# Optimization experiments

Hardware: AMD Instinct MI355X
Metric: run time of the kernel (lower is better)

The kernel has to match this reference:

```python
import jax, jax.numpy as jnp
import numpy as np

N, C, H, W = 8, 32, 16, 16   # input batch / channels / spatial
OC = 64                       # out_channels
K = 3                         # kernel_size
PAD = 1                       # padding (stride=1, dilation=1 -> output HxW == input HxW)
WIDTH = 8                     # hwcfg['width']
RLEN = 2 ** WIDTH             # Sobol RNG sequence length = 256
CKK = C * K * K               # unfolded patch length = 288
B = N * H * W                 # flattened patch batch = 2048


def _sobol_rng():
    # 1-D Sobol sequence == van der Corput base-2: bit-reversed counter scaled to [0, 2^width)
    idx = np.arange(RLEN, dtype=np.uint32)
    rev = np.zeros(RLEN, dtype=np.uint32)
    for b in range(WIDTH):
        rev |= ((idx >> b) & 1) << (WIDTH - 1 - b)
    return jnp.asarray(rev.astype(np.float32))


def setup_inputs() -> dict:
    key = jax.random.key(0)
    k1, k2, k3, k4, k5, k6 = jax.random.split(key, 6)
    # unary (stochastic bitstream) input: bits in {0,1}
    x = jax.random.bernoulli(k1, 0.5, (N, C, H, W)).astype(jnp.float32)
    # BinGen, bipolar: binary = round((v + 1)/2 * 2^width), v in [-1, 1]
    w = jax.random.uniform(k2, (OC, CKK), minval=-1.0, maxval=1.0)
    w_bin = jnp.round((w + 1.0) / 2.0 * RLEN)
    b = jax.random.uniform(k3, (OC,), minval=-1.0, maxval=1.0)
    b_bin = jnp.round((b + 1.0) / 2.0 * RLEN)
    rng = _sobol_rng()
    # mid-stream BSGen index state (per patch position, as the module cats to batch copies)
    wrdx_i1 = jax.random.randint(k4, (B, OC, CKK), 0, RLEN, dtype=jnp.int32)
    wrdx_i0 = jax.random.randint(k5, (B, OC, CKK), 0, RLEN, dtype=jnp.int32)
    brdx = jax.random.randint(k6, (OC,), 0, RLEN, dtype=jnp.int32)
    return {"x": x, "w_bin": w_bin, "b_bin": b_bin, "rng": rng,
            "wrdx_i1": wrdx_i1, "wrdx_i0": wrdx_i0, "brdx": brdx}


def _unfold(x):
    # even cycle -> ConstantPad2d(pad, 0); torch.nn.functional.unfold ordering (c, kh, kw)
    xp = jnp.pad(x, ((0, 0), (0, 0), (PAD, PAD), (PAD, PAD)))
    cols = jnp.stack([xp[:, :, i:i + H, j:j + W] for i in range(K) for j in range(K)], axis=2)
    # [N, C, K*K, H, W] -> [N, CKK, L] -> [N, L, CKK] -> [B, CKK]
    return cols.reshape(N, CKK, H * W).transpose(0, 2, 1).reshape(B, CKK)


def reference(x, w_bin, b_bin, rng, wrdx_i1, wrdx_i0, brdx):
    ib1 = _unfold(x)                                                        # [B, CKK], bits
    # BSGen: bit = (binary_value > rng[index % RLEN])
    wbit1 = (w_bin[None] > rng[wrdx_i1 % RLEN]).astype(jnp.float32)         # [B, OC, CKK]
    wbit0 = 1.0 - (w_bin[None] > rng[wrdx_i0 % RLEN]).astype(jnp.float32)   # [B, OC, CKK]
    # bipolar parallel counter: x*w1 path + (1-x)*(1-w) path
    obin = (jnp.einsum('bk,bok->bo', ib1, wbit1)
            + jnp.einsum('bk,bok->bo', 1.0 - ib1, wbit0))                   # [B, OC]
    bbit = (b_bin > rng[brdx % RLEN]).astype(jnp.float32)                   # [OC]
    # fold(1,1): [N, L, OC] -> [N, OC, H, W]
    out = obin.reshape(N, H * W, OC).transpose(0, 2, 1).reshape(N, OC, H, W)
    return out + bbit[None, :, None, None]
```

## Files before the change

### kernel.cpp

```cpp
#include <hip/hip_runtime.h>


#define CH   32
#define HH   16
#define WW   16
#define OCN  64
#define CKK  288
#define LL   256
#define BB   2048

#define WS_XM_OFF 0
#define WS_WK_OFF 131072
#define WS_BB_OFF 204800

__device__ __forceinline__ float unf_val(const float* __restrict__ x,
                                         int n, int h, int w0, int k) {
    int c  = k / 9;
    int r  = k - c * 9;
    int kh = r / 3;
    int kw = r - kh * 3;
    int ih = h + kh - 1;
    int iw = w0 + kw - 1;
    float v = 0.f;
    if ((unsigned)ih < 16u && (unsigned)iw < 16u)
        v = x[((n * CH + c) * HH + ih) * WW + iw];
    return v;
}

__global__ __launch_bounds__(256) void fsu_pre(
    const float* __restrict__ x, const float* __restrict__ w_bin,
    const float* __restrict__ b_bin, const int* __restrict__ brdx,
    unsigned long long* __restrict__ xm, unsigned* __restrict__ wk,
    float* __restrict__ bb)
{
    if (blockIdx.x == 512) {
        for (int i = threadIdx.x; i < OCN * CKK; i += 256) {
            unsigned wi = (unsigned)w_bin[i];
            wk[i] = (wi >= 256u) ? 0xFFFFFFFFu : (wi << 24);
        }
        if (threadIdx.x < OCN) {
            int o = threadIdx.x;
            float rv = (float)(__brev((unsigned)brdx[o]) >> 24);
            bb[o] = (b_bin[o] > rv) ? 1.f : 0.f;
        }
        return;
    }
    const int wave = threadIdx.x >> 6;
    const int lane = threadIdx.x & 63;
    const int b = blockIdx.x * 4 + wave;
    const int n = b >> 8, l = b & 255;
    const int h = l >> 4, w0 = l & 15;

    unsigned long long m[8];
    #pragma unroll
    for (int e = 0; e < 4; ++e)
        m[e] = __ballot(unf_val(x, n, h, w0, lane * 4 + e) != 0.f);
    #pragma unroll
    for (int e = 0; e < 4; ++e)
        m[4 + e] = __ballot(unf_val(x, n, h, w0, 256 + (lane & 7) * 4 + e) != 0.f);

    if (lane == 0) {
        #pragma unroll
        for (int e = 0; e < 8; ++e) xm[(size_t)b * 8 + e] = m[e];
    }
}

struct Row {
    int4  a, c;
    uint4 k;
    int4  at, ct;
    uint4 kt;
};

__device__ __forceinline__ void load_row(Row& r, const int* __restrict__ p1,
                                         const int* __restrict__ p0,
                                         const unsigned* __restrict__ pw,
                                         int j, int lane, int tl) {
    const int4*  q1 = (const int4*)(p1 + j * CKK);
    const int4*  q0 = (const int4*)(p0 + j * CKK);
    const uint4* qw = (const uint4*)(pw + j * CKK);
    r.a  = q1[lane]; r.c  = q0[lane]; r.k  = qw[lane];
    r.at = q1[tl];   r.ct = q0[tl];   r.kt = qw[tl];
}

__device__ __forceinline__ unsigned long long chunkm(unsigned k, int a1, int a0,
                                                     unsigned long long xm) {
    unsigned long long m1 = __ballot(k > __brev((unsigned)a1));
    unsigned long long m0 = __ballot(k > __brev((unsigned)a0));
    return (xm & m1) | (~xm & ~m0);
}

__global__ __launch_bounds__(256) void fsu_stream(
    const int* __restrict__ wrdx1, const int* __restrict__ wrdx0,
    const unsigned* __restrict__ wk, const unsigned long long* __restrict__ xm,
    const float* __restrict__ bb, float* __restrict__ out)
{
    const int blk  = blockIdx.x;
    const int b    = blk >> 2;
    const int og   = blk & 3;
    const int wave = threadIdx.x >> 6;
    const int lane = threadIdx.x & 63;
    const int obase = og * 16 + wave * 4;
    const int n = b >> 8, l = b & 255;
    const int tl = 64 + (lane & 7);

    const unsigned long long* xb = xm + (size_t)b * 8;
    const unsigned long long xm0 = xb[0], xm1 = xb[1], xm2 = xb[2], xm3 = xb[3];
    const unsigned long long xt0 = xb[4], xt1 = xb[5], xt2 = xb[6], xt3 = xb[7];

    const int* p1 = wrdx1 + ((size_t)b * OCN + obase) * CKK;
    const int* p0 = wrdx0 + ((size_t)b * OCN + obase) * CKK;
    const unsigned* pw = wk + (size_t)obase * CKK;
    float* po = out + ((size_t)n * OCN + obase) * LL + l;

    auto docompute = [&](const Row& r, int j) {
        unsigned cnt = 0;
        cnt += __popcll(chunkm(r.k.x,  r.a.x,  r.c.x,  xm0));
        cnt += __popcll(chunkm(r.k.y,  r.a.y,  r.c.y,  xm1));
        cnt += __popcll(chunkm(r.k.z,  r.a.z,  r.c.z,  xm2));
        cnt += __popcll(chunkm(r.k.w,  r.a.w,  r.c.w,  xm3));
        cnt += __popcll(chunkm(r.kt.x, r.at.x, r.ct.x, xt0) & 0xFFull);
        cnt += __popcll(chunkm(r.kt.y, r.at.y, r.ct.y, xt1) & 0xFFull);
        cnt += __popcll(chunkm(r.kt.z, r.at.z, r.ct.z, xt2) & 0xFFull);
        cnt += __popcll(chunkm(r.kt.w, r.at.w, r.ct.w, xt3) & 0xFFull);
        if (lane == 0)
            po[j * LL] = (float)cnt + bb[obase + j];
    };

    Row A, B;
    load_row(A, p1, p0, pw, 0, lane, tl);
    load_row(B, p1, p0, pw, 1, lane, tl);
    __builtin_amdgcn_sched_barrier(0);
    docompute(A, 0);
    load_row(A, p1, p0, pw, 2, lane, tl);
    __builtin_amdgcn_sched_barrier(0);
    docompute(B, 1);
    load_row(B, p1, p0, pw, 3, lane, tl);
    __builtin_amdgcn_sched_barrier(0);
    docompute(A, 2);
    docompute(B, 3);
}

extern "C" void kernel_launch(void* const* d_in, const int* in_sizes, int n_in,
                              void* d_out, int out_size, void* d_ws, size_t ws_size,
                              hipStream_t stream) {
    const float* x     = (const float*)d_in[0];
    const float* w_bin = (const float*)d_in[1];
    const float* b_bin = (const float*)d_in[2];
    const int*   wrdx1 = (const int*)d_in[4];
    const int*   wrdx0 = (const int*)d_in[5];
    const int*   brdx  = (const int*)d_in[6];
    float*       out   = (float*)d_out;

    unsigned long long* xm = (unsigned long long*)((char*)d_ws + WS_XM_OFF);
    unsigned*           wk = (unsigned*)((char*)d_ws + WS_WK_OFF);
    float*              bb = (float*)((char*)d_ws + WS_BB_OFF);

    fsu_pre<<<dim3(513), dim3(256), 0, stream>>>(x, w_bin, b_bin, brdx, xm, wk, bb);
    fsu_stream<<<dim3(BB * 4), dim3(256), 0, stream>>>(wrdx1, wrdx0, wk, xm, bb, out);
}
```

Baseline: 330.2 us.

## Stream index rows via async global-to-LDS loads with per-wave double buffering

Reorganises fsu_stream so each wave owns one output channel and iterates over 16 patches. Weight keys and the bias bit are computed once in registers, and the index rows are streamed into LDS through global_load_lds with a two-buffer pipeline gated by vmcnt waits. The weight and bias preprocessing moves out of fsu_pre, and the grid shrinks from 8192 to 2048 blocks. The aim is to overlap HBM loads of the large wrdx arrays with the ballot and popcount work and to cut per-block setup, at the cost of hand-tuned waitcnt ordering and fewer resident blocks.

```diff
diff --git a/kernel.cpp b/kernel.cpp
--- a/kernel.cpp
+++ b/kernel.cpp
@@ -8,10 +8,25 @@
 #define CKK  288
 #define LL   256
 #define BB   2048
+#define BPW  16
+#define ROWSTRIDE (OCN * CKK)
 
-#define WS_XM_OFF 0
-#define WS_WK_OFF 131072
-#define WS_BB_OFF 204800
+__device__ __forceinline__ unsigned wkey(float wv) {
+    unsigned wi = (unsigned)wv;
+    return (wi >= 256u) ? 0xFFFFFFFFu : (wi << 24);
+}
+
+__device__ __forceinline__ void async16(const void* g, void* l) {
+    __builtin_amdgcn_global_load_lds(
+        (const __attribute__((address_space(1))) void*)g,
+        (__attribute__((address_space(3))) void*)l, 16, 0, 0);
+}
+
+__device__ __forceinline__ unsigned long long rfl64(unsigned long long v) {
+    unsigned lo = __builtin_amdgcn_readfirstlane((unsigned)v);
+    unsigned hi = __builtin_amdgcn_readfirstlane((unsigned)(v >> 32));
+    return ((unsigned long long)hi << 32) | lo;
+}
 
 __device__ __forceinline__ float unf_val(const float* __restrict__ x,
                                          int n, int h, int w0, int k) {
@@ -28,23 +43,8 @@
 }
 
 __global__ __launch_bounds__(256) void fsu_pre(
-    const float* __restrict__ x, const float* __restrict__ w_bin,
-    const float* __restrict__ b_bin, const int* __restrict__ brdx,
-    unsigned long long* __restrict__ xm, unsigned* __restrict__ wk,
-    float* __restrict__ bb)
+    const float* __restrict__ x, unsigned long long* __restrict__ xm)
 {
-    if (blockIdx.x == 512) {
-        for (int i = threadIdx.x; i < OCN * CKK; i += 256) {
-            unsigned wi = (unsigned)w_bin[i];
-            wk[i] = (wi >= 256u) ? 0xFFFFFFFFu : (wi << 24);
-        }
-        if (threadIdx.x < OCN) {
-            int o = threadIdx.x;
-            float rv = (float)(__brev((unsigned)brdx[o]) >> 24);
-            bb[o] = (b_bin[o] > rv) ? 1.f : 0.f;
-        }
-        return;
-    }
     const int wave = threadIdx.x >> 6;
     const int lane = threadIdx.x & 63;
     const int b = blockIdx.x * 4 + wave;
@@ -65,24 +65,6 @@
     }
 }
 
-struct Row {
-    int4  a, c;
-    uint4 k;
-    int4  at, ct;
-    uint4 kt;
-};
-
-__device__ __forceinline__ void load_row(Row& r, const int* __restrict__ p1,
-                                         const int* __restrict__ p0,
-                                         const unsigned* __restrict__ pw,
-                                         int j, int lane, int tl) {
-    const int4*  q1 = (const int4*)(p1 + j * CKK);
-    const int4*  q0 = (const int4*)(p0 + j * CKK);
-    const uint4* qw = (const uint4*)(pw + j * CKK);
-    r.a  = q1[lane]; r.c  = q0[lane]; r.k  = qw[lane];
-    r.at = q1[tl];   r.ct = q0[tl];   r.kt = qw[tl];
-}
-
 __device__ __forceinline__ unsigned long long chunkm(unsigned k, int a1, int a0,
                                                      unsigned long long xm) {
     unsigned long long m1 = __ballot(k > __brev((unsigned)a1));
@@ -92,53 +74,97 @@
 
 __global__ __launch_bounds__(256) void fsu_stream(
     const int* __restrict__ wrdx1, const int* __restrict__ wrdx0,
-    const unsigned* __restrict__ wk, const unsigned long long* __restrict__ xm,
-    const float* __restrict__ bb, float* __restrict__ out)
+    const float* __restrict__ w_bin, const float* __restrict__ b_bin,
+    const int* __restrict__ brdx,
+    const unsigned long long* __restrict__ xm,
+    float* __restrict__ out)
 {
-    const int blk  = blockIdx.x;
-    const int b    = blk >> 2;
-    const int og   = blk & 3;
+    __shared__ __align__(16) int buf[4][2][2 * CKK];
+    __shared__ __align__(16) unsigned long long xml[BPW * 8];
+
     const int wave = threadIdx.x >> 6;
     const int lane = threadIdx.x & 63;
-    const int obase = og * 16 + wave * 4;
-    const int n = b >> 8, l = b & 255;
-    const int tl = 64 + (lane & 7);
+    const int og   = blockIdx.x & 15;
+    const int bch  = blockIdx.x >> 4;
+    const int o    = og * 4 + wave;
+    const int b0   = bch * BPW;
 
-    const unsigned long long* xb = xm + (size_t)b * 8;
-    const unsigned long long xm0 = xb[0], xm1 = xb[1], xm2 = xb[2], xm3 = xb[3];
-    const unsigned long long xt0 = xb[4], xt1 = xb[5], xt2 = xb[6], xt3 = xb[7];
+    const float* pw = w_bin + (size_t)o * CKK;
+    float4 wm = ((const float4*)pw)[lane];
+    float4 wt = ((const float4*)pw)[64 + (lane & 7)];
+    uint4 km = make_uint4(wkey(wm.x), wkey(wm.y), wkey(wm.z), wkey(wm.w));
+    uint4 kt = make_uint4(wkey(wt.x), wkey(wt.y), wkey(wt.z), wkey(wt.w));
+    float bbv = (b_bin[o] > (float)(__brev((unsigned)brdx[o]) >> 24)) ? 1.f : 0.f;
 
-    const int* p1 = wrdx1 + ((size_t)b * OCN + obase) * CKK;
-    const int* p0 = wrdx0 + ((size_t)b * OCN + obase) * CKK;
-    const unsigned* pw = wk + (size_t)obase * CKK;
-    float* po = out + ((size_t)n * OCN + obase) * LL + l;
+    if (wave == 0)
+        async16((const char*)(xm + (size_t)b0 * 8) + lane * 16,
+                (char*)xml);
+    __syncthreads();
 
-    auto docompute = [&](const Row& r, int j) {
-        unsigned cnt = 0;
-        cnt += __popcll(chunkm(r.k.x,  r.a.x,  r.c.x,  xm0));
-        cnt += __popcll(chunkm(r.k.y,  r.a.y,  r.c.y,  xm1));
-        cnt += __popcll(chunkm(r.k.z,  r.a.z,  r.c.z,  xm2));
-        cnt += __popcll(chunkm(r.k.w,  r.a.w,  r.c.w,  xm3));
-        cnt += __popcll(chunkm(r.kt.x, r.at.x, r.ct.x, xt0) & 0xFFull);
-        cnt += __popcll(chunkm(r.kt.y, r.at.y, r.ct.y, xt1) & 0xFFull);
-        cnt += __popcll(chunkm(r.kt.z, r.at.z, r.ct.z, xt2) & 0xFFull);
-        cnt += __popcll(chunkm(r.kt.w, r.at.w, r.ct.w, xt3) & 0xFFull);
-        if (lane == 0)
-            po[j * LL] = (float)cnt + bb[obase + j];
+    int* bufA = &buf[wave][0][0];
+    int* bufB = &buf[wave][1][0];
+
+    const int* g1 = wrdx1 + ((size_t)b0 * OCN + o) * CKK + lane * 4;
+    const int* g0 = wrdx0 + ((size_t)b0 * OCN + o) * CKK + lane * 4;
+    const int* t1 = wrdx1 + ((size_t)b0 * OCN + o) * CKK + 256 + (lane & 7) * 4;
+    const int* t0 = wrdx0 + ((size_t)b0 * OCN + o) * CKK + 256 + (lane & 7) * 4;
+
+    auto issue = [&](int j, int* dst) {
+        __builtin_amdgcn_sched_barrier(0);
+        async16(g1 + (size_t)j * ROWSTRIDE, dst);
+        async16(g0 + (size_t)j * ROWSTRIDE, dst + CKK);
+        if (lane < 8) {
+            async16(t1 + (size_t)j * ROWSTRIDE, (char*)dst + 1024);
+            async16(t0 + (size_t)j * ROWSTRIDE, (char*)dst + 4 * CKK + 1024);
+        }
     };
 
-    Row A, B;
-    load_row(A, p1, p0, pw, 0, lane, tl);
-    load_row(B, p1, p0, pw, 1, lane, tl);
-    __builtin_amdgcn_sched_barrier(0);
-    docompute(A, 0);
-    load_row(A, p1, p0, pw, 2, lane, tl);
-    __builtin_amdgcn_sched_barrier(0);
-    docompute(B, 1);
-    load_row(B, p1, p0, pw, 3, lane, tl);
-    __builtin_amdgcn_sched_barrier(0);
-    docompute(A, 2);
-    docompute(B, 3);
+    auto compute = [&](const int* src, int j) {
+        const unsigned long long* xr = xml + j * 8;
+        unsigned long long x0 = rfl64(xr[0]), x1 = rfl64(xr[1]);
+        unsigned long long x2 = rfl64(xr[2]), x3 = rfl64(xr[3]);
+        unsigned long long y0 = rfl64(xr[4]), y1 = rfl64(xr[5]);
+        unsigned long long y2 = rfl64(xr[6]), y3 = rfl64(xr[7]);
+
+        int4 a  = *(const int4*)((const char*)src + lane * 16);
+        int4 at = *(const int4*)((const char*)src + 1024 + (lane & 7) * 16);
+        int4 c  = *(const int4*)((const char*)src + 4 * CKK + lane * 16);
+        int4 ct = *(const int4*)((const char*)src + 4 * CKK + 1024 + (lane & 7) * 16);
+
+        unsigned cnt = 0;
+        cnt += __popcll(chunkm(km.x, a.x, c.x, x0));
+        cnt += __popcll(chunkm(km.y, a.y, c.y, x1));
+        cnt += __popcll(chunkm(km.z, a.z, c.z, x2));
+        cnt += __popcll(chunkm(km.w, a.w, c.w, x3));
+        cnt += __popcll(chunkm(kt.x, at.x, ct.x, y0) & 0xFFull);
+        cnt += __popcll(chunkm(kt.y, at.y, ct.y, y1) & 0xFFull);
+        cnt += __popcll(chunkm(kt.z, at.z, ct.z, y2) & 0xFFull);
+        cnt += __popcll(chunkm(kt.w, at.w, ct.w, y3) & 0xFFull);
+
+        if (lane == 0) {
+            int bcur = b0 + j;
+            int n = bcur >> 8, l = bcur & 255;
+            out[((size_t)n * OCN + o) * LL + l] = (float)cnt + bbv;
+        }
+    };
+
+    issue(0, bufA);
+    #pragma unroll
+    for (int p = 0; p < 8; ++p) {
+        const int j = p * 2;
+        issue(j + 1, bufB);
+        asm volatile("s_waitcnt vmcnt(4)" ::: "memory");
+        __builtin_amdgcn_sched_barrier(0);
+        compute(bufA, j);
+        if (p < 7) {
+            issue(j + 2, bufA);
+            asm volatile("s_waitcnt vmcnt(4)" ::: "memory");
+        } else {
+            asm volatile("s_waitcnt vmcnt(0)" ::: "memory");
+        }
+        __builtin_amdgcn_sched_barrier(0);
+        compute(bufB, j + 1);
+    }
 }
 
 extern "C" void kernel_launch(void* const* d_in, const int* in_sizes, int n_in,
@@ -152,10 +178,9 @@
     const int*   brdx  = (const int*)d_in[6];
     float*       out   = (float*)d_out;
 
-    unsigned long long* xm = (unsigned long long*)((char*)d_ws + WS_XM_OFF);
-    unsigned*           wk = (unsigned*)((char*)d_ws + WS_WK_OFF);
-    float*              bb = (float*)((char*)d_ws + WS_BB_OFF);
+    unsigned long long* xm = (unsigned long long*)d_ws;
 
-    fsu_pre<<<dim3(513), dim3(256), 0, stream>>>(x, w_bin, b_bin, brdx, xm, wk, bb);
-    fsu_stream<<<dim3(BB * 4), dim3(256), 0, stream>>>(wrdx1, wrdx0, wk, xm, bb, out);
+    fsu_pre<<<dim3(BB / 4), dim3(256), 0, stream>>>(x, xm);
+    fsu_stream<<<dim3(BB), dim3(256), 0, stream>>>(wrdx1, wrdx0, w_bin, b_bin,
+                                                   brdx, xm, out);
 }
```

New measurement: 324.5 us. No clear change (-1.7%).

## Stream index rows through LDS with async global-to-LDS loads, one block per patch

Applied to the files above, without the earlier changes.

The streaming kernel now runs one block per patch, with each wave handling 16 output channels. Index rows are staged into LDS with global_load_lds in a 4-deep ring buffer, and s_waitcnt vmcnt controls when each slot is read. Weights are stored as 16-bit values and copied once per block into LDS, and the comparison moves to the 8-bit domain. The goal is to keep more bytes in flight on what is a bandwidth-bound read of two 150MB index tensors, at the cost of larger LDS use and fragile hand-written waitcnt accounting.

```diff
diff --git a/kernel.cpp b/kernel.cpp
--- a/kernel.cpp
+++ b/kernel.cpp
@@ -6,12 +6,20 @@
 #define WW   16
 #define OCN  64
 #define CKK  288
+#define CKKB 1152
 #define LL   256
 #define BB   2048
+#define DEPTH 4
 
 #define WS_XM_OFF 0
 #define WS_WK_OFF 131072
-#define WS_BB_OFF 204800
+#define WS_BB_OFF 167936
+
+__device__ __forceinline__ void async16(const void* g, void* l) {
+    __builtin_amdgcn_global_load_lds(
+        (const __attribute__((address_space(1))) void*)g,
+        (__attribute__((address_space(3))) void*)l, 16, 0, 0);
+}
 
 __device__ __forceinline__ float unf_val(const float* __restrict__ x,
                                          int n, int h, int w0, int k) {
@@ -30,14 +38,12 @@
 __global__ __launch_bounds__(256) void fsu_pre(
     const float* __restrict__ x, const float* __restrict__ w_bin,
     const float* __restrict__ b_bin, const int* __restrict__ brdx,
-    unsigned long long* __restrict__ xm, unsigned* __restrict__ wk,
+    unsigned long long* __restrict__ xm, unsigned short* __restrict__ wk16,
     float* __restrict__ bb)
 {
     if (blockIdx.x == 512) {
-        for (int i = threadIdx.x; i < OCN * CKK; i += 256) {
-            unsigned wi = (unsigned)w_bin[i];
-            wk[i] = (wi >= 256u) ? 0xFFFFFFFFu : (wi << 24);
-        }
+        for (int i = threadIdx.x; i < OCN * CKK; i += 256)
+            wk16[i] = (unsigned short)(unsigned)w_bin[i];
         if (threadIdx.x < OCN) {
             int o = threadIdx.x;
             float rv = (float)(__brev((unsigned)brdx[o]) >> 24);
@@ -65,80 +71,97 @@
     }
 }
 
-struct Row {
-    int4  a, c;
-    uint4 k;
-    int4  at, ct;
-    uint4 kt;
-};
-
-__device__ __forceinline__ void load_row(Row& r, const int* __restrict__ p1,
-                                         const int* __restrict__ p0,
-                                         const unsigned* __restrict__ pw,
-                                         int j, int lane, int tl) {
-    const int4*  q1 = (const int4*)(p1 + j * CKK);
-    const int4*  q0 = (const int4*)(p0 + j * CKK);
-    const uint4* qw = (const uint4*)(pw + j * CKK);
-    r.a  = q1[lane]; r.c  = q0[lane]; r.k  = qw[lane];
-    r.at = q1[tl];   r.ct = q0[tl];   r.kt = qw[tl];
-}
-
 __device__ __forceinline__ unsigned long long chunkm(unsigned k, int a1, int a0,
-                                                     unsigned long long xm) {
-    unsigned long long m1 = __ballot(k > __brev((unsigned)a1));
-    unsigned long long m0 = __ballot(k > __brev((unsigned)a0));
-    return (xm & m1) | (~xm & ~m0);
+                                                     unsigned long long xm_) {
+    unsigned long long m1 = __ballot(k > (__brev((unsigned)a1) >> 24));
+    unsigned long long m0 = __ballot(k > (__brev((unsigned)a0) >> 24));
+    return (xm_ & m1) | (~xm_ & ~m0);
 }
 
 __global__ __launch_bounds__(256) void fsu_stream(
     const int* __restrict__ wrdx1, const int* __restrict__ wrdx0,
-    const unsigned* __restrict__ wk, const unsigned long long* __restrict__ xm,
+    const unsigned short* __restrict__ wk16,
+    const unsigned long long* __restrict__ xm,
     const float* __restrict__ bb, float* __restrict__ out)
 {
-    const int blk  = blockIdx.x;
-    const int b    = blk >> 2;
-    const int og   = blk & 3;
+    __shared__ __align__(16) unsigned short wkl[OCN * CKK];
+    __shared__ __align__(16) char buf[4][DEPTH][2 * CKKB];
+
     const int wave = threadIdx.x >> 6;
     const int lane = threadIdx.x & 63;
-    const int obase = og * 16 + wave * 4;
+    const int b = blockIdx.x;
     const int n = b >> 8, l = b & 255;
-    const int tl = 64 + (lane & 7);
+    const int r0 = b * 64 + wave * 16;
+    const int o0 = wave * 16;
+
+    {
+        const char* src = (const char*)wk16 + (size_t)(wave * 9) * 1024
+                        + (size_t)lane * 16;
+        char* dst = (char*)wkl + wave * 9 * 1024;
+        #pragma unroll
+        for (int i = 0; i < 9; ++i)
+            async16(src + i * 1024, dst + i * 1024);
+    }
+
+    const char* s1 = (const char*)wrdx1 + (size_t)r0 * CKKB;
+    const char* s0 = (const char*)wrdx0 + (size_t)r0 * CKKB;
+
+    auto issue = [&](int j, int d) {
+        char* dstb = &buf[wave][d][0];
+        const char* r1 = s1 + (size_t)j * CKKB;
+        const char* rq = s0 + (size_t)j * CKKB;
+        async16(r1 + lane * 16, dstb);
+        async16(rq + lane * 16, dstb + CKKB);
+        if (lane < 8) {
+            async16(r1 + 1024 + lane * 16, dstb + 1024);
+            async16(rq + 1024 + lane * 16, dstb + CKKB + 1024);
+        }
+    };
+
+    issue(0, 0); issue(1, 1); issue(2, 2); issue(3, 3);
 
     const unsigned long long* xb = xm + (size_t)b * 8;
-    const unsigned long long xm0 = xb[0], xm1 = xb[1], xm2 = xb[2], xm3 = xb[3];
-    const unsigned long long xt0 = xb[4], xt1 = xb[5], xt2 = xb[6], xt3 = xb[7];
+    const unsigned long long x0 = xb[0], x1 = xb[1], x2 = xb[2], x3 = xb[3];
+    const unsigned long long y0 = xb[4], y1 = xb[5], y2 = xb[6], y3 = xb[7];
 
-    const int* p1 = wrdx1 + ((size_t)b * OCN + obase) * CKK;
-    const int* p0 = wrdx0 + ((size_t)b * OCN + obase) * CKK;
-    const unsigned* pw = wk + (size_t)obase * CKK;
-    float* po = out + ((size_t)n * OCN + obase) * LL + l;
+    asm volatile("s_waitcnt vmcnt(12)" ::: "memory");
+    __builtin_amdgcn_s_barrier();
+    __builtin_amdgcn_sched_barrier(0);
 
-    auto docompute = [&](const Row& r, int j) {
+    #pragma unroll
+    for (int j = 0; j < 16; ++j) {
+        if (j <= 12)      asm volatile("s_waitcnt vmcnt(12)" ::: "memory");
+        else if (j == 13) asm volatile("s_waitcnt vmcnt(8)"  ::: "memory");
+        else if (j == 14) asm volatile("s_waitcnt vmcnt(4)"  ::: "memory");
+        else              asm volatile("s_waitcnt vmcnt(0)"  ::: "memory");
+        __builtin_amdgcn_sched_barrier(0);
+
+        const char* src = &buf[wave][j & 3][0];
+        const int o = o0 + j;
+        const unsigned short* wkr = wkl + o * CKK;
+
+        uint2 km = *(const uint2*)((const char*)wkr + lane * 8);
+        uint2 kt = *(const uint2*)((const char*)wkr + 512 + (lane & 7) * 8);
+        int4 a  = *(const int4*)(src + lane * 16);
+        int4 c  = *(const int4*)(src + CKKB + lane * 16);
+        int4 at = *(const int4*)(src + 1024 + (lane & 7) * 16);
+        int4 ct = *(const int4*)(src + CKKB + 1024 + (lane & 7) * 16);
+
+        if (j + 4 < 16) issue(j + 4, (j + 4) & 3);
+
         unsigned cnt = 0;
-        cnt += __popcll(chunkm(r.k.x,  r.a.x,  r.c.x,  xm0));
-        cnt += __popcll(chunkm(r.k.y,  r.a.y,  r.c.y,  xm1));
-        cnt += __popcll(chunkm(r.k.z,  r.a.z,  r.c.z,  xm2));
-        cnt += __popcll(chunkm(r.k.w,  r.a.w,  r.c.w,  xm3));
-        cnt += __popcll(chunkm(r.kt.x, r.at.x, r.ct.x, xt0) & 0xFFull);
-        cnt += __popcll(chunkm(r.kt.y, r.at.y, r.ct.y, xt1) & 0xFFull);
-        cnt += __popcll(chunkm(r.kt.z, r.at.z, r.ct.z, xt2) & 0xFFull);
-        cnt += __popcll(chunkm(r.kt.w, r.at.w, r.ct.w, xt3) & 0xFFull);
+        cnt += __popcll(chunkm(km.x & 0xFFFFu, a.x,  c.x,  x0));
+        cnt += __popcll(chunkm(km.x >> 16,     a.y,  c.y,  x1));
+        cnt += __popcll(chunkm(km.y & 0xFFFFu, a.z,  c.z,  x2));
+        cnt += __popcll(chunkm(km.y >> 16,     a.w,  c.w,  x3));
+        cnt += __popcll(chunkm(kt.x & 0xFFFFu, at.x, ct.x, y0) & 0xFFull);
+        cnt += __popcll(chunkm(kt.x >> 16,     at.y, ct.y, y1) & 0xFFull);
+        cnt += __popcll(chunkm(kt.y & 0xFFFFu, at.z, ct.z, y2) & 0xFFull);
+        cnt += __popcll(chunkm(kt.y >> 16,     at.w, ct.w, y3) & 0xFFull);
+
         if (lane == 0)
-            po[j * LL] = (float)cnt + bb[obase + j];
-    };
-
-    Row A, B;
-    load_row(A, p1, p0, pw, 0, lane, tl);
-    load_row(B, p1, p0, pw, 1, lane, tl);
-    __builtin_amdgcn_sched_barrier(0);
-    docompute(A, 0);
-    load_row(A, p1, p0, pw, 2, lane, tl);
-    __builtin_amdgcn_sched_barrier(0);
-    docompute(B, 1);
-    load_row(B, p1, p0, pw, 3, lane, tl);
-    __builtin_amdgcn_sched_barrier(0);
-    docompute(A, 2);
-    docompute(B, 3);
+            out[((size_t)n * OCN + o) * LL + l] = (float)cnt + bb[o];
+    }
 }
 
 extern "C" void kernel_launch(void* const* d_in, const int* in_sizes, int n_in,
@@ -153,9 +176,11 @@
     float*       out   = (float*)d_out;
 
     unsigned long long* xm = (unsigned long long*)((char*)d_ws + WS_XM_OFF);
-    unsigned*           wk = (unsigned*)((char*)d_ws + WS_WK_OFF);
+    unsigned short*   wk16 = (unsigned short*)((char*)d_ws + WS_WK_OFF);
     float*              bb = (float*)((char*)d_ws + WS_BB_OFF);
 
-    fsu_pre<<<dim3(513), dim3(256), 0, stream>>>(x, w_bin, b_bin, brdx, xm, wk, bb);
-    fsu_stream<<<dim3(BB * 4), dim3(256), 0, stream>>>(wrdx1, wrdx0, wk, xm, bb, out);
+    fsu_pre<<<dim3(513), dim3(256), 0, stream>>>(x, w_bin, b_bin, brdx,
+                                                 xm, wk16, bb);
+    fsu_stream<<<dim3(BB), dim3(256), 0, stream>>>(wrdx1, wrdx0, wk16, xm,
+                                                   bb, out);
 }
```

Result: slower. 338.9 us (+2.6%).
